# Kernel optimization log

Hardware: AMD Instinct MI355X
Metric: run time of the kernel (lower is better)

Reference implementation:

```python
import jax, jax.numpy as jnp
import numpy as np

B, S, H = 4, 2048, 1024
E, K = 8, 2

def setup_inputs() -> dict:
    key = jax.random.key(0)
    ks = jax.random.split(key, 5)
    scale = 1.0 / np.sqrt(H)
    return {
        "x": jax.random.normal(ks[0], (B, S, H), dtype=jnp.float32),
        "router_w": jax.random.uniform(ks[1], (E, H), jnp.float32, -scale, scale),
        "router_b": jax.random.uniform(ks[2], (E,), jnp.float32, -scale, scale),
        "expert_w": jax.random.uniform(ks[3], (E, H, H), jnp.float32, -scale, scale),
        "expert_b": jax.random.uniform(ks[4], (E, H), jnp.float32, -scale, scale),
    }


def reference(x, router_w, router_b, expert_w, expert_b):
    # Router: [b,s,E]
    scores = jnp.einsum("bsh,eh->bse", x, router_w) + router_b
    probs = jax.nn.softmax(scores, axis=-1)
    p, expert_id = jax.lax.top_k(probs, K)          # [b,s,K]
    # Renormalize top-k probs (matches p / p.sum(dim=2))
    p = p / jnp.sum(p, axis=-1, keepdims=True)
    # Per-token combine weight per expert: [b,s,E]
    onehot = jax.nn.one_hot(expert_id, E, dtype=x.dtype)  # [b,s,K,E]
    w_comb = jnp.einsum("bske,bsk->bse", onehot, p)
    # All-expert linear (Linear: x @ W.T + b): [b,s,E,h]
    all_out = jnp.einsum("bsh,edh->bsed", x, expert_w) + expert_b
    # Weighted combine over selected experts: [b,s,h]
    return jnp.einsum("bse,bsed->bsd", w_comb, all_out)
```

## Files before the change

kernel.cpp:

```cpp
#include <hip/hip_runtime.h>
#include <hip/hip_bf16.h>
#include <math.h>

#define TOK 8192
#define HD 1024
#define NE 8
#define SLOTS 17408
#define MAXTILES 136

typedef _Float16 half8 __attribute__((ext_vector_type(8)));
typedef _Float16 half4v __attribute__((ext_vector_type(4)));
typedef float floatx4 __attribute__((ext_vector_type(4)));

__global__ void moe_score(const float* __restrict__ x,
                          const float* __restrict__ rw,
                          const float* __restrict__ rb,
                          int* __restrict__ epair,
                          float* __restrict__ w1out,
                          _Float16* __restrict__ xh) {
  const int lane = threadIdx.x & 63;
  const int wid = threadIdx.x >> 6;
  const int t = blockIdx.x * 4 + wid;
  const float4* xp = (const float4*)(x + (size_t)t * HD);
  float4 xr[4];
#pragma unroll
  for (int i = 0; i < 4; ++i) xr[i] = xp[lane + 64 * i];
  if (xh) {
    _Float16* xo = xh + (size_t)t * HD;
#pragma unroll
    for (int i = 0; i < 4; ++i) {
      half4v h = {(_Float16)xr[i].x, (_Float16)xr[i].y,
                  (_Float16)xr[i].z, (_Float16)xr[i].w};
      *(half4v*)(xo + (lane + 64 * i) * 4) = h;
    }
  }
  float sc[NE];
#pragma unroll
  for (int e = 0; e < NE; ++e) {
    const float4* wp = (const float4*)(rw + e * HD);
    float a = 0.f;
#pragma unroll
    for (int i = 0; i < 4; ++i) {
      float4 w = wp[lane + 64 * i];
      a += xr[i].x * w.x + xr[i].y * w.y + xr[i].z * w.z + xr[i].w * w.w;
    }
#pragma unroll
    for (int off = 32; off > 0; off >>= 1) a += __shfl_xor(a, off);
    sc[e] = a + rb[e];
  }
  float b1 = sc[0]; int e1 = 0;
#pragma unroll
  for (int e = 1; e < NE; ++e) if (sc[e] > b1) { b1 = sc[e]; e1 = e; }
  float b2 = -1e30f; int e2 = 0;
#pragma unroll
  for (int e = 0; e < NE; ++e) { if (e != e1 && sc[e] > b2) { b2 = sc[e]; e2 = e; } }
  if (lane == 0) {
    epair[t] = e1 | (e2 << 8);
    w1out[t] = 1.f / (1.f + expf(b2 - b1));
  }
}

__global__ __launch_bounds__(1024) void moe_count1(
    const int* __restrict__ epair,
    int* __restrict__ cntp,
    int* __restrict__ cnt2,
    int* __restrict__ basep,
    int* __restrict__ tile_map) {
  __shared__ int lc[NE];
  const int tid = threadIdx.x;
  if (tid < NE) lc[tid] = 0;
  __syncthreads();
  int c[NE];
#pragma unroll
  for (int e = 0; e < NE; ++e) c[e] = 0;
#pragma unroll
  for (int i = 0; i < TOK / 1024; ++i) {
    int ep = epair[tid + 1024 * i];
    int e1 = ep & 0xff, e2 = ep >> 8;
#pragma unroll
    for (int e = 0; e < NE; ++e) c[e] += (e1 == e) + (e2 == e);
  }
#pragma unroll
  for (int e = 0; e < NE; ++e) {
#pragma unroll
    for (int off = 32; off > 0; off >>= 1) c[e] += __shfl_xor(c[e], off);
    if ((tid & 63) == 0) atomicAdd(&lc[e], c[e]);
  }
  __syncthreads();
  if (tid == 0) {
    int b = 0, nt = 0;
    for (int e = 0; e < NE; ++e) {
      int ce = lc[e];
      cntp[e * 64] = ce;
      basep[e] = b;
      cnt2[e * 64] = b;
      int mt = (ce + 127) >> 7;
      for (int m = 0; m < mt; ++m) tile_map[nt++] = (e << 16) | m;
      b += (ce + 127) & ~127;
    }
    for (; nt < MAXTILES; ++nt) tile_map[nt] = -1;
  }
}

__global__ void moe_scatter(const int* __restrict__ epair,
                            const float* __restrict__ w1in,
                            int* __restrict__ cnt2,
                            int* __restrict__ tok_list,
                            float* __restrict__ tok_w,
                            int* __restrict__ slot_of) {
  __shared__ int lcnt[NE];
  __shared__ int lbase[NE];
  const int tid = threadIdx.x;
  const int t = blockIdx.x * 256 + tid;
  if (tid < NE) lcnt[tid] = 0;
  __syncthreads();
  int ep = epair[t];
  int e1 = ep & 0xff, e2 = ep >> 8;
  float w1 = w1in[t];
  int o1 = atomicAdd(&lcnt[e1], 1);
  int o2 = atomicAdd(&lcnt[e2], 1);
  __syncthreads();
  if (tid < NE) lbase[tid] = atomicAdd(&cnt2[tid * 64], lcnt[tid]);
  __syncthreads();
  int s1 = lbase[e1] + o1;
  tok_list[s1] = t; tok_w[s1] = w1; slot_of[2 * t] = s1;
  int s2 = lbase[e2] + o2;
  tok_list[s2] = t; tok_w[s2] = 1.f - w1; slot_of[2 * t + 1] = s2;
}

__global__ void cvt_f32_f16(const float* __restrict__ src,
                            _Float16* __restrict__ dst, int n4) {
  int i = blockIdx.x * 256 + threadIdx.x;
  if (i >= n4) return;
  float4 v = ((const float4*)src)[i];
  half4v h = {(_Float16)v.x, (_Float16)v.y, (_Float16)v.z, (_Float16)v.w};
  ((half4v*)dst)[i] = h;
}

template <int EPI>
__global__ __launch_bounds__(256) void moe_gemm(
    const _Float16* __restrict__ Ah, const _Float16* __restrict__ Bh,
    const float* __restrict__ eb,
    const int* __restrict__ tile_map, const int* __restrict__ cntp,
    const int* __restrict__ base,
    const int* __restrict__ tok_list, const float* __restrict__ tok_w,
    _Float16* __restrict__ scratch, float* __restrict__ out) {
  const int tm = tile_map[blockIdx.x >> 3];
  if (tm < 0) return;
  const int e = tm >> 16;
  const int m0 = (tm & 0xffff) << 7;
  const int ce = cntp[e * 64];
  const int sbase = base[e];
  const int n0 = (blockIdx.x & 7) << 7;
  const int tid = threadIdx.x;
  const int lane = tid & 63;
  const int wid = tid >> 6;
  const int wm = wid & 1, wn = wid >> 1;

  __shared__ _Float16 A_s[128 * 64];
  __shared__ _Float16 B_s[128 * 64];
  __shared__ int tok_s[128];
  __shared__ float w_s[128];

  if (tid < 128) {
    int tk = 0; float w = 0.f;
    if (m0 + tid < ce) { tk = tok_list[sbase + m0 + tid]; w = tok_w[sbase + m0 + tid]; }
    tok_s[tid] = tk; w_s[tid] = w;
  }
  __syncthreads();

  floatx4 acc[4][4];
  floatx4 zero = {0.f, 0.f, 0.f, 0.f};
#pragma unroll
  for (int i = 0; i < 4; ++i)
#pragma unroll
    for (int j = 0; j < 4; ++j) acc[i][j] = zero;

  const size_t wbase = (size_t)e * HD * HD;
  const int rloc = lane >> 3, sub = lane & 7;
  const int csw = (sub ^ rloc) * 8;
  size_t agbase[4], bgbase[4];
#pragma unroll
  for (int q = 0; q < 4; ++q) {
    int row = wid * 32 + q * 8 + rloc;
    agbase[q] = (size_t)tok_s[row] * HD + csw;
    bgbase[q] = wbase + (size_t)(n0 + row) * HD + csw;
  }
  const int x7 = lane & 7, q4 = lane >> 4;

  for (int k0 = 0; k0 < HD; k0 += 64) {
#pragma unroll
    for (int q = 0; q < 4; ++q) {
      const int r0 = wid * 32 + q * 8;
      __builtin_amdgcn_global_load_lds(
          (const __attribute__((address_space(1))) unsigned int*)(Ah + agbase[q] + k0),
          (__attribute__((address_space(3))) unsigned int*)&A_s[r0 * 64], 16, 0, 0);
      __builtin_amdgcn_global_load_lds(
          (const __attribute__((address_space(1))) unsigned int*)(Bh + bgbase[q] + k0),
          (__attribute__((address_space(3))) unsigned int*)&B_s[r0 * 64], 16, 0, 0);
    }
    __syncthreads();
#pragma unroll
    for (int kf = 0; kf < 2; ++kf) {
      half8 afr[4], bfr[4];
      const int cc = kf * 4 + q4;
#pragma unroll
      for (int i = 0; i < 4; ++i)
        afr[i] = *(const half8*)&A_s[(wm * 64 + i * 16 + (lane & 15)) * 64 + ((cc ^ x7) * 8)];
#pragma unroll
      for (int j = 0; j < 4; ++j)
        bfr[j] = *(const half8*)&B_s[(wn * 64 + j * 16 + (lane & 15)) * 64 + ((cc ^ x7) * 8)];
#pragma unroll
      for (int i = 0; i < 4; ++i)
#pragma unroll
        for (int j = 0; j < 4; ++j)
          acc[i][j] = __builtin_amdgcn_mfma_f32_16x16x32_f16(afr[i], bfr[j], acc[i][j], 0, 0, 0);
    }
    __syncthreads();
  }

#pragma unroll
  for (int j = 0; j < 4; ++j) {
    int col = n0 + wn * 64 + j * 16 + (lane & 15);
    float bias = eb[e * HD + col];
#pragma unroll
    for (int i = 0; i < 4; ++i) {
      int rbase = wm * 64 + i * 16 + (q4 << 2);
#pragma unroll
      for (int r = 0; r < 4; ++r) {
        int row = rbase + r;
        float v = w_s[row] * (acc[i][j][r] + bias);
        if (EPI == 1) {
          scratch[(size_t)(sbase + m0 + row) * HD + col] = (_Float16)v;
        } else {
          if (m0 + row < ce)
            atomicAdd(&out[(size_t)tok_s[row] * HD + col], v);
        }
      }
    }
  }
}

__global__ void moe_combine(const _Float16* __restrict__ scratch,
                            const int* __restrict__ slot_of,
                            float* __restrict__ out) {
  const int tid = threadIdx.x;
  const int t = blockIdx.x * 2 + (tid >> 7);
  const int c = (tid & 127) * 8;
  int sa = slot_of[2 * t], sb = slot_of[2 * t + 1];
  half8 a = *(const half8*)&scratch[(size_t)sa * HD + c];
  half8 b = *(const half8*)&scratch[(size_t)sb * HD + c];
  float* o = out + (size_t)t * HD + c;
  float4 o0 = {(float)a[0] + (float)b[0], (float)a[1] + (float)b[1],
               (float)a[2] + (float)b[2], (float)a[3] + (float)b[3]};
  float4 o1 = {(float)a[4] + (float)b[4], (float)a[5] + (float)b[5],
               (float)a[6] + (float)b[6], (float)a[7] + (float)b[7]};
  *(float4*)o = o0;
  *(float4*)(o + 4) = o1;
}

extern "C" void kernel_launch(void* const* d_in, const int* in_sizes, int n_in,
                              void* d_out, int out_size, void* d_ws, size_t ws_size,
                              hipStream_t stream) {
  (void)in_sizes; (void)n_in;
  const float* x  = (const float*)d_in[0];
  const float* rw = (const float*)d_in[1];
  const float* rb = (const float*)d_in[2];
  const float* ew = (const float*)d_in[3];
  const float* eb = (const float*)d_in[4];
  float* out = (float*)d_out;

  char* w = (char*)d_ws;
  int*   cntp     = (int*)(w + 0);
  int*   cnt2     = (int*)(w + 2048);
  int*   basep    = (int*)(w + 4096);
  int*   tile_map = (int*)(w + 4160);
  int*   tok_list = (int*)(w + 4800);
  float* tok_w    = (float*)(w + 4800 + SLOTS * 4);
  size_t off = 4800 + 2ull * SLOTS * 4;
  int*   epair    = (int*)(w + off);  off += TOK * 4;
  int*   slot_of  = (int*)(w + off);  off += TOK * 8;
  float* w1buf    = (float*)(w + off); off += TOK * 4;
  off = (off + 255) & ~255ull;
  size_t xh_off = off;
  size_t wh_off = xh_off + (size_t)TOK * HD * 2;
  size_t scr_off = wh_off + (size_t)NE * HD * HD * 2;
  size_t needscr = scr_off + (size_t)SLOTS * HD * 2;
  bool fast16 = ws_size >= scr_off;
  bool fastscr = ws_size >= needscr;

  if (!fastscr)
    hipMemsetAsync(d_out, 0, (size_t)out_size * sizeof(float), stream);

  _Float16* xh = fast16 ? (_Float16*)(w + xh_off) : nullptr;
  _Float16* wh = fast16 ? (_Float16*)(w + wh_off) : nullptr;
  _Float16* scr = fastscr ? (_Float16*)(w + scr_off) : nullptr;

  moe_score<<<TOK / 4, 256, 0, stream>>>(x, rw, rb, epair, w1buf, xh);
  moe_count1<<<1, 1024, 0, stream>>>(epair, cntp, cnt2, basep, tile_map);
  moe_scatter<<<TOK / 256, 256, 0, stream>>>(epair, w1buf, cnt2, tok_list, tok_w, slot_of);

  if (fast16) {
    int n4w = NE * HD * HD / 4;
    cvt_f32_f16<<<(n4w + 255) / 256, 256, 0, stream>>>(ew, wh, n4w);
    if (fastscr) {
      moe_gemm<1><<<MAXTILES * 8, 256, 0, stream>>>(
          xh, wh, eb, tile_map, cntp, basep, tok_list, tok_w, scr, out);
      moe_combine<<<TOK / 2, 256, 0, stream>>>(scr, slot_of, out);
    } else {
      moe_gemm<0><<<MAXTILES * 8, 256, 0, stream>>>(
          xh, wh, eb, tile_map, cntp, basep, tok_list, tok_w, nullptr, out);
    }
  } else {
    moe_gemm<0><<<MAXTILES * 8, 256, 0, stream>>>(
        (const _Float16*)x, (const _Float16*)ew, eb, tile_map, cntp, basep,
        tok_list, tok_w, nullptr, out);
  }
}
```

Before: 209.9 us.

## Fuse routing, counting, scatter and weight conversion into one cooperative kernel

Replaces the separate score, count, scatter and weight-conversion kernels with one cooperative kernel of 256 blocks. Each block routes 32 tokens, keeps a per-block expert histogram and converts a slice of expert weights to fp16. After a grid-wide sync it computes prefix offsets from the histograms and writes the token lists. The GEMM now uses a 3D grid (n-tile, m-tile, expert) with early exit in place of a tile map. The aim is to cut launch overhead and intermediate buffers, at the cost of a grid sync, 256-block-only parallelism for the routing work, and many empty GEMM blocks launched.

```diff
diff --git a/kernel.cpp b/kernel.cpp
--- a/kernel.cpp
+++ b/kernel.cpp
@@ -1,157 +1,156 @@
 #include <hip/hip_runtime.h>
 #include <hip/hip_bf16.h>
+#include <hip/hip_cooperative_groups.h>
 #include <math.h>
+
+namespace cg = cooperative_groups;
 
 #define TOK 8192
 #define HD 1024
 #define NE 8
 #define SLOTS 17408
-#define MAXTILES 136
 
 typedef _Float16 half8 __attribute__((ext_vector_type(8)));
 typedef _Float16 half4v __attribute__((ext_vector_type(4)));
 typedef float floatx4 __attribute__((ext_vector_type(4)));
 
-__global__ void moe_score(const float* __restrict__ x,
-                          const float* __restrict__ rw,
-                          const float* __restrict__ rb,
-                          int* __restrict__ epair,
-                          float* __restrict__ w1out,
-                          _Float16* __restrict__ xh) {
-  const int lane = threadIdx.x & 63;
-  const int wid = threadIdx.x >> 6;
-  const int t = blockIdx.x * 4 + wid;
-  const float4* xp = (const float4*)(x + (size_t)t * HD);
-  float4 xr[4];
-#pragma unroll
-  for (int i = 0; i < 4; ++i) xr[i] = xp[lane + 64 * i];
-  if (xh) {
+__global__ void fused_router(const float* __restrict__ x,
+                             const float* __restrict__ rw,
+                             const float* __restrict__ rb,
+                             const float* __restrict__ ew,
+                             _Float16* __restrict__ xh,
+                             _Float16* __restrict__ wh,
+                             int* __restrict__ hist,
+                             int* __restrict__ cntp,
+                             int* __restrict__ basep,
+                             int* __restrict__ tok_list,
+                             float* __restrict__ tok_w,
+                             int* __restrict__ slot_of) {
+  const int tid = threadIdx.x;
+  const int lane = tid & 63;
+  const int wid = tid >> 6;
+  const int blk = blockIdx.x;
+
+  __shared__ int hcnt[NE];
+  __shared__ int tokE1[32], tokE2[32];
+  __shared__ float tokW1[32];
+  __shared__ int ebase_s[NE], etot_s[NE], alloc_s[NE];
+
+  if (tid < NE) hcnt[tid] = 0;
+  __syncthreads();
+
+  for (int i = 0; i < 8; ++i) {
+    const int li = wid * 8 + i;
+    const int t = blk * 32 + li;
+    const float4* xp = (const float4*)(x + (size_t)t * HD);
+    float4 xr[4];
+#pragma unroll
+    for (int k = 0; k < 4; ++k) xr[k] = xp[lane + 64 * k];
     _Float16* xo = xh + (size_t)t * HD;
 #pragma unroll
-    for (int i = 0; i < 4; ++i) {
-      half4v h = {(_Float16)xr[i].x, (_Float16)xr[i].y,
-                  (_Float16)xr[i].z, (_Float16)xr[i].w};
-      *(half4v*)(xo + (lane + 64 * i) * 4) = h;
-    }
-  }
-  float sc[NE];
-#pragma unroll
-  for (int e = 0; e < NE; ++e) {
-    const float4* wp = (const float4*)(rw + e * HD);
-    float a = 0.f;
-#pragma unroll
-    for (int i = 0; i < 4; ++i) {
-      float4 w = wp[lane + 64 * i];
-      a += xr[i].x * w.x + xr[i].y * w.y + xr[i].z * w.z + xr[i].w * w.w;
-    }
-#pragma unroll
-    for (int off = 32; off > 0; off >>= 1) a += __shfl_xor(a, off);
-    sc[e] = a + rb[e];
-  }
-  float b1 = sc[0]; int e1 = 0;
-#pragma unroll
-  for (int e = 1; e < NE; ++e) if (sc[e] > b1) { b1 = sc[e]; e1 = e; }
-  float b2 = -1e30f; int e2 = 0;
-#pragma unroll
-  for (int e = 0; e < NE; ++e) { if (e != e1 && sc[e] > b2) { b2 = sc[e]; e2 = e; } }
+    for (int k = 0; k < 4; ++k) {
+      half4v h = {(_Float16)xr[k].x, (_Float16)xr[k].y,
+                  (_Float16)xr[k].z, (_Float16)xr[k].w};
+      *(half4v*)(xo + (lane + 64 * k) * 4) = h;
+    }
+    float sc[NE];
+#pragma unroll
+    for (int e = 0; e < NE; ++e) {
+      const float4* wp = (const float4*)(rw + e * HD);
+      float a = 0.f;
+#pragma unroll
+      for (int k = 0; k < 4; ++k) {
+        float4 w = wp[lane + 64 * k];
+        a += xr[k].x * w.x + xr[k].y * w.y + xr[k].z * w.z + xr[k].w * w.w;
+      }
+#pragma unroll
+      for (int off = 32; off > 0; off >>= 1) a += __shfl_xor(a, off);
+      sc[e] = a + rb[e];
+    }
+    float b1 = sc[0]; int e1 = 0;
+#pragma unroll
+    for (int e = 1; e < NE; ++e) if (sc[e] > b1) { b1 = sc[e]; e1 = e; }
+    float b2 = -1e30f; int e2 = 0;
+#pragma unroll
+    for (int e = 0; e < NE; ++e) { if (e != e1 && sc[e] > b2) { b2 = sc[e]; e2 = e; } }
+    if (lane == 0) {
+      tokE1[li] = e1; tokE2[li] = e2;
+      tokW1[li] = 1.f / (1.f + expf(b2 - b1));
+      atomicAdd(&hcnt[e1], 1);
+      atomicAdd(&hcnt[e2], 1);
+    }
+  }
+  {
+    const int g = blk * 256 + tid;
+    const float4* src = (const float4*)ew;
+    half4v* dst = (half4v*)wh;
+#pragma unroll
+    for (int j = 0; j < 32; ++j) {
+      float4 v = src[g + 65536 * j];
+      half4v h = {(_Float16)v.x, (_Float16)v.y, (_Float16)v.z, (_Float16)v.w};
+      dst[g + 65536 * j] = h;
+    }
+  }
+  __syncthreads();
+  if (tid < NE) hist[tid * 256 + blk] = hcnt[tid];
+
+  cg::this_grid().sync();
+
+#pragma unroll
+  for (int eo = 0; eo < 2; ++eo) {
+    const int e = wid + eo * 4;
+    int s_prev = 0, s_tot = 0;
+#pragma unroll
+    for (int j = 0; j < 4; ++j) {
+      int b = lane + 64 * j;
+      int h = hist[e * 256 + b];
+      s_tot += h;
+      s_prev += (b < blk) ? h : 0;
+    }
+#pragma unroll
+    for (int off = 32; off > 0; off >>= 1) {
+      s_prev += __shfl_xor(s_prev, off);
+      s_tot += __shfl_xor(s_tot, off);
+    }
+    if (lane == 0) { ebase_s[e] = s_prev; etot_s[e] = s_tot; }
+  }
+  __syncthreads();
+  if (tid == 0) {
+    int b = 0;
+    for (int e = 0; e < NE; ++e) {
+      alloc_s[e] = b + ebase_s[e];
+      if (blk == 0) { cntp[e * 64] = etot_s[e]; basep[e] = b; }
+      b += (etot_s[e] + 127) & ~127;
+    }
+  }
+  __syncthreads();
   if (lane == 0) {
-    epair[t] = e1 | (e2 << 8);
-    w1out[t] = 1.f / (1.f + expf(b2 - b1));
-  }
-}
-
-__global__ __launch_bounds__(1024) void moe_count1(
-    const int* __restrict__ epair,
-    int* __restrict__ cntp,
-    int* __restrict__ cnt2,
-    int* __restrict__ basep,
-    int* __restrict__ tile_map) {
-  __shared__ int lc[NE];
-  const int tid = threadIdx.x;
-  if (tid < NE) lc[tid] = 0;
-  __syncthreads();
-  int c[NE];
-#pragma unroll
-  for (int e = 0; e < NE; ++e) c[e] = 0;
-#pragma unroll
-  for (int i = 0; i < TOK / 1024; ++i) {
-    int ep = epair[tid + 1024 * i];
-    int e1 = ep & 0xff, e2 = ep >> 8;
-#pragma unroll
-    for (int e = 0; e < NE; ++e) c[e] += (e1 == e) + (e2 == e);
-  }
-#pragma unroll
-  for (int e = 0; e < NE; ++e) {
-#pragma unroll
-    for (int off = 32; off > 0; off >>= 1) c[e] += __shfl_xor(c[e], off);
-    if ((tid & 63) == 0) atomicAdd(&lc[e], c[e]);
-  }
-  __syncthreads();
-  if (tid == 0) {
-    int b = 0, nt = 0;
-    for (int e = 0; e < NE; ++e) {
-      int ce = lc[e];
-      cntp[e * 64] = ce;
-      basep[e] = b;
-      cnt2[e * 64] = b;
-      int mt = (ce + 127) >> 7;
-      for (int m = 0; m < mt; ++m) tile_map[nt++] = (e << 16) | m;
-      b += (ce + 127) & ~127;
-    }
-    for (; nt < MAXTILES; ++nt) tile_map[nt] = -1;
-  }
-}
-
-__global__ void moe_scatter(const int* __restrict__ epair,
-                            const float* __restrict__ w1in,
-                            int* __restrict__ cnt2,
-                            int* __restrict__ tok_list,
-                            float* __restrict__ tok_w,
-                            int* __restrict__ slot_of) {
-  __shared__ int lcnt[NE];
-  __shared__ int lbase[NE];
-  const int tid = threadIdx.x;
-  const int t = blockIdx.x * 256 + tid;
-  if (tid < NE) lcnt[tid] = 0;
-  __syncthreads();
-  int ep = epair[t];
-  int e1 = ep & 0xff, e2 = ep >> 8;
-  float w1 = w1in[t];
-  int o1 = atomicAdd(&lcnt[e1], 1);
-  int o2 = atomicAdd(&lcnt[e2], 1);
-  __syncthreads();
-  if (tid < NE) lbase[tid] = atomicAdd(&cnt2[tid * 64], lcnt[tid]);
-  __syncthreads();
-  int s1 = lbase[e1] + o1;
-  tok_list[s1] = t; tok_w[s1] = w1; slot_of[2 * t] = s1;
-  int s2 = lbase[e2] + o2;
-  tok_list[s2] = t; tok_w[s2] = 1.f - w1; slot_of[2 * t + 1] = s2;
-}
-
-__global__ void cvt_f32_f16(const float* __restrict__ src,
-                            _Float16* __restrict__ dst, int n4) {
-  int i = blockIdx.x * 256 + threadIdx.x;
-  if (i >= n4) return;
-  float4 v = ((const float4*)src)[i];
-  half4v h = {(_Float16)v.x, (_Float16)v.y, (_Float16)v.z, (_Float16)v.w};
-  ((half4v*)dst)[i] = h;
+    for (int i = 0; i < 8; ++i) {
+      const int li = wid * 8 + i;
+      const int t = blk * 32 + li;
+      int e1 = tokE1[li], e2 = tokE2[li];
+      float w1 = tokW1[li];
+      int s1 = atomicAdd(&alloc_s[e1], 1);
+      tok_list[s1] = t; tok_w[s1] = w1; slot_of[2 * t] = s1;
+      int s2 = atomicAdd(&alloc_s[e2], 1);
+      tok_list[s2] = t; tok_w[s2] = 1.f - w1; slot_of[2 * t + 1] = s2;
+    }
+  }
 }
 
 template <int EPI>
 __global__ __launch_bounds__(256) void moe_gemm(
     const _Float16* __restrict__ Ah, const _Float16* __restrict__ Bh,
     const float* __restrict__ eb,
-    const int* __restrict__ tile_map, const int* __restrict__ cntp,
-    const int* __restrict__ base,
+    const int* __restrict__ cntp, const int* __restrict__ base,
     const int* __restrict__ tok_list, const float* __restrict__ tok_w,
     _Float16* __restrict__ scratch, float* __restrict__ out) {
-  const int tm = tile_map[blockIdx.x >> 3];
-  if (tm < 0) return;
-  const int e = tm >> 16;
-  const int m0 = (tm & 0xffff) << 7;
+  const int e = blockIdx.z;
   const int ce = cntp[e * 64];
+  const int m0 = blockIdx.y << 7;
+  if (m0 >= ce) return;
   const int sbase = base[e];
-  const int n0 = (blockIdx.x & 7) << 7;
+  const int n0 = blockIdx.x << 7;
   const int tid = threadIdx.x;
   const int lane = tid & 63;
   const int wid = tid >> 6;
@@ -272,48 +271,42 @@
 
   char* w = (char*)d_ws;
   int*   cntp     = (int*)(w + 0);
-  int*   cnt2     = (int*)(w + 2048);
-  int*   basep    = (int*)(w + 4096);
-  int*   tile_map = (int*)(w + 4160);
-  int*   tok_list = (int*)(w + 4800);
-  float* tok_w    = (float*)(w + 4800 + SLOTS * 4);
-  size_t off = 4800 + 2ull * SLOTS * 4;
-  int*   epair    = (int*)(w + off);  off += TOK * 4;
-  int*   slot_of  = (int*)(w + off);  off += TOK * 8;
-  float* w1buf    = (float*)(w + off); off += TOK * 4;
+  int*   basep    = (int*)(w + 2048);
+  int*   hist     = (int*)(w + 2304);
+  size_t off = 2304 + NE * 256 * 4;
+  int*   tok_list = (int*)(w + off);  off += (size_t)SLOTS * 4;
+  float* tok_w    = (float*)(w + off); off += (size_t)SLOTS * 4;
+  int*   slot_of  = (int*)(w + off);  off += (size_t)TOK * 8;
   off = (off + 255) & ~255ull;
   size_t xh_off = off;
   size_t wh_off = xh_off + (size_t)TOK * HD * 2;
   size_t scr_off = wh_off + (size_t)NE * HD * HD * 2;
   size_t needscr = scr_off + (size_t)SLOTS * HD * 2;
-  bool fast16 = ws_size >= scr_off;
   bool fastscr = ws_size >= needscr;
 
   if (!fastscr)
     hipMemsetAsync(d_out, 0, (size_t)out_size * sizeof(float), stream);
 
-  _Float16* xh = fast16 ? (_Float16*)(w + xh_off) : nullptr;
-  _Float16* wh = fast16 ? (_Float16*)(w + wh_off) : nullptr;
+  _Float16* xh = (_Float16*)(w + xh_off);
+  _Float16* wh = (_Float16*)(w + wh_off);
   _Float16* scr = fastscr ? (_Float16*)(w + scr_off) : nullptr;
 
-  moe_score<<<TOK / 4, 256, 0, stream>>>(x, rw, rb, epair, w1buf, xh);
-  moe_count1<<<1, 1024, 0, stream>>>(epair, cntp, cnt2, basep, tile_map);
-  moe_scatter<<<TOK / 256, 256, 0, stream>>>(epair, w1buf, cnt2, tok_list, tok_w, slot_of);
-
-  if (fast16) {
-    int n4w = NE * HD * HD / 4;
-    cvt_f32_f16<<<(n4w + 255) / 256, 256, 0, stream>>>(ew, wh, n4w);
-    if (fastscr) {
-      moe_gemm<1><<<MAXTILES * 8, 256, 0, stream>>>(
-          xh, wh, eb, tile_map, cntp, basep, tok_list, tok_w, scr, out);
-      moe_combine<<<TOK / 2, 256, 0, stream>>>(scr, slot_of, out);
-    } else {
-      moe_gemm<0><<<MAXTILES * 8, 256, 0, stream>>>(
-          xh, wh, eb, tile_map, cntp, basep, tok_list, tok_w, nullptr, out);
-    }
+  {
+    void* args[] = {(void*)&x, (void*)&rw, (void*)&rb, (void*)&ew,
+                    (void*)&xh, (void*)&wh, (void*)&hist,
+                    (void*)&cntp, (void*)&basep,
+                    (void*)&tok_list, (void*)&tok_w, (void*)&slot_of};
+    hipLaunchCooperativeKernel((void*)fused_router, dim3(256), dim3(256),
+                               args, 0, stream);
+  }
+
+  dim3 grid(HD / 128, TOK / 128, NE);
+  if (fastscr) {
+    moe_gemm<1><<<grid, 256, 0, stream>>>(xh, wh, eb, cntp, basep,
+                                          tok_list, tok_w, scr, out);
+    moe_combine<<<TOK / 2, 256, 0, stream>>>(scr, slot_of, out);
   } else {
-    moe_gemm<0><<<MAXTILES * 8, 256, 0, stream>>>(
-        (const _Float16*)x, (const _Float16*)ew, eb, tile_map, cntp, basep,
-        tok_list, tok_w, nullptr, out);
+    moe_gemm<0><<<grid, 256, 0, stream>>>(xh, wh, eb, cntp, basep,
+                                          tok_list, tok_w, nullptr, out);
   }
 }
```

Result: slower. 283.6 us (+35.1%).
